# Kernel tuning notes

Hardware: AMD Instinct MI355X
Metric: run time of the kernel (lower is better)

Reference implementation:

```python
import jax, jax.numpy as jnp
import numpy as np

N_NODES = 50000
N_EDGES = 300000
HEADS = 2
OUT_CH = 128
BN_EPS = 1e-5
NEG_SLOPE = 0.2


def _batchnorm(x, g, b):
    # training-mode BatchNorm1d: biased batch statistics
    mean = x.mean(axis=0)
    var = x.var(axis=0)
    return (x - mean) * jax.lax.rsqrt(var + BN_EPS) * g + b


def _gatv2(x, src, dst, edge_attr, Wl, bl, Wr, br, We, att, bias, concat):
    # PyG GATv2Conv, share_weights=False, aggr='add'
    n = x.shape[0]
    xl = (x @ Wl + bl).reshape(n, HEADS, OUT_CH)  # source messages
    xr = (x @ Wr + br).reshape(n, HEADS, OUT_CH)  # destination term
    ee = (edge_attr @ We).reshape(-1, HEADS, OUT_CH)
    s = jax.nn.leaky_relu(xl[src] + xr[dst] + ee, NEG_SLOPE)  # [E,H,C]
    alpha = jnp.einsum('ehc,hc->eh', s, att)  # [E,H]
    # segment softmax over edges grouped by destination node
    m = jax.ops.segment_max(alpha, dst, num_segments=n)
    a = jnp.exp(alpha - m[dst])
    den = jax.ops.segment_sum(a, dst, num_segments=n)
    a = a / (den[dst] + 1e-16)
    out = jax.ops.segment_sum(xl[src] * a[:, :, None], dst, num_segments=n)  # [N,H,C]
    out = out.reshape(n, HEADS * OUT_CH) if concat else out.mean(axis=1)
    return out + bias


def setup_inputs() -> dict:
    key = jax.random.key(0)
    ks = jax.random.split(key, 16)
    d = {}
    d['h'] = jax.random.normal(ks[0], (N_NODES, 5), jnp.float32)
    d['edge_index'] = jax.random.randint(ks[1], (2, N_EDGES), 0, N_NODES, jnp.int64)
    d['edge_weight'] = jax.random.uniform(ks[2], (N_EDGES, 1), jnp.float32)
    d['bn0_g'] = jnp.ones((5,), jnp.float32)
    d['bn0_b'] = jnp.zeros((5,), jnp.float32)
    d['bn1_g'] = jnp.ones((256,), jnp.float32)
    d['bn1_b'] = jnp.zeros((256,), jnp.float32)
    def lin(k, fan_in, fan_out):
        return jax.random.normal(k, (fan_in, fan_out), jnp.float32) * (1.0 / np.sqrt(fan_in))
    # conv1: in=5 -> heads*out=256, concat=True
    d['c1_Wl'] = lin(ks[3], 5, 256); d['c1_bl'] = jnp.zeros((256,), jnp.float32)
    d['c1_Wr'] = lin(ks[4], 5, 256); d['c1_br'] = jnp.zeros((256,), jnp.float32)
    d['c1_We'] = lin(ks[5], 1, 256)
    d['c1_att'] = jax.random.normal(ks[6], (HEADS, OUT_CH), jnp.float32) * 0.1
    d['c1_bias'] = jnp.zeros((256,), jnp.float32)
    # mu: in=256 -> 128, concat=False
    d['mu_Wl'] = lin(ks[7], 256, 256); d['mu_bl'] = jnp.zeros((256,), jnp.float32)
    d['mu_Wr'] = lin(ks[8], 256, 256); d['mu_br'] = jnp.zeros((256,), jnp.float32)
    d['mu_We'] = lin(ks[9], 1, 256)
    d['mu_att'] = jax.random.normal(ks[10], (HEADS, OUT_CH), jnp.float32) * 0.1
    d['mu_bias'] = jnp.zeros((128,), jnp.float32)
    # log_std: same shapes as mu
    d['ls_Wl'] = lin(ks[11], 256, 256); d['ls_bl'] = jnp.zeros((256,), jnp.float32)
    d['ls_Wr'] = lin(ks[12], 256, 256); d['ls_br'] = jnp.zeros((256,), jnp.float32)
    d['ls_We'] = lin(ks[13], 1, 256)
    d['ls_att'] = jax.random.normal(ks[14], (HEADS, OUT_CH), jnp.float32) * 0.1
    d['ls_bias'] = jnp.zeros((128,), jnp.float32)
    return d


def reference(h, edge_index, edge_weight, bn0_g, bn0_b, bn1_g, bn1_b,
              c1_Wl, c1_bl, c1_Wr, c1_br, c1_We, c1_att, c1_bias,
              mu_Wl, mu_bl, mu_Wr, mu_br, mu_We, mu_att, mu_bias,
              ls_Wl, ls_bl, ls_Wr, ls_br, ls_We, ls_att, ls_bias):
    src, dst = edge_index[0], edge_index[1]
    x = _batchnorm(h, bn0_g, bn0_b)
    x = _gatv2(x, src, dst, edge_weight, c1_Wl, c1_bl, c1_Wr, c1_br, c1_We, c1_att, c1_bias, concat=True)
    x = jax.nn.relu(_batchnorm(x, bn1_g, bn1_b))
    # dropout identity (eval / deterministic)
    mu = _gatv2(x, src, dst, edge_weight, mu_Wl, mu_bl, mu_Wr, mu_br, mu_We, mu_att, mu_bias, concat=False)
    log_std = _gatv2(x, src, dst, edge_weight, ls_Wl, ls_bl, ls_Wr, ls_br, ls_We, ls_att, ls_bias, concat=False)
    return (mu, log_std)
```

## Files before the change

### kernel.cpp

```cpp
#include <hip/hip_runtime.h>
#include <math.h>

#define N_NODES 50000
#define N_EDGES 300000
#define BN_EPS 1e-5f
#define NEG_SLOPE 0.2f

#define RB_COUNT 3128
#define SCAN_TILES 49
#define BN1_BLOCKS 523
#define K5_BLOCKS 1024

typedef short bf8v __attribute__((ext_vector_type(8)));
typedef float f4v __attribute__((ext_vector_type(4)));
typedef float f2v __attribute__((ext_vector_type(2)));

__device__ inline unsigned short f2bf(float f) {
    union { float f; unsigned u; } c; c.f = f;
    unsigned r = c.u + 0x7fffu + ((c.u >> 16) & 1u);
    return (unsigned short)(r >> 16);
}

__device__ inline f2v bfpair(unsigned u) {
    union { unsigned u; float f; } lo, hi;
    lo.u = u << 16;
    hi.u = u & 0xffff0000u;
    f2v r; r.x = lo.f; r.y = hi.f;
    return r;
}

__device__ inline void async_copy16(void* lds, const void* g) {
    __builtin_amdgcn_global_load_lds(
        (const __attribute__((address_space(1))) unsigned int*)g,
        (__attribute__((address_space(3))) unsigned int*)lds, 16, 0, 0);
}

__global__ void bn0_reduce(const float* __restrict__ h, float* __restrict__ acc ) {
    __shared__ float lds[4][10];
    int tid = threadIdx.x;
    int lane = tid & 63, wave = tid >> 6;
    float ls[5] = {0,0,0,0,0}, lq[5] = {0,0,0,0,0};
    for (int r = blockIdx.x * 256 + tid; r < N_NODES; r += 128 * 256) {
        #pragma unroll
        for (int k = 0; k < 5; k++) {
            float v = h[r*5 + k];
            ls[k] += v; lq[k] += v*v;
        }
    }
    #pragma unroll
    for (int k = 0; k < 5; k++) {
        #pragma unroll
        for (int m = 1; m <= 32; m <<= 1) {
            ls[k] += __shfl_xor(ls[k], m, 64);
            lq[k] += __shfl_xor(lq[k], m, 64);
        }
    }
    if (lane == 0) {
        #pragma unroll
        for (int k = 0; k < 5; k++) { lds[wave][k] = ls[k]; lds[wave][5+k] = lq[k]; }
    }
    __syncthreads();
    if (tid < 10) {
        float s = lds[0][tid] + lds[1][tid] + lds[2][tid] + lds[3][tid];
        atomicAdd(&acc[tid], s);
    }
}

__global__ void edge_count(const int* __restrict__ dst, int* __restrict__ count) {
    int e = blockIdx.x * blockDim.x + threadIdx.x;
    if (e < N_EDGES) atomicAdd(&count[dst[e]], 1);
}

__global__ void local_scan(const int* __restrict__ count, int* __restrict__ offsets,
                           int* __restrict__ tileSum) {
    __shared__ int lds[1024];
    int tid = threadIdx.x;
    int i = blockIdx.x * 1024 + tid;
    int v = (i < N_NODES) ? count[i] : 0;
    lds[tid] = v;
    __syncthreads();
    #pragma unroll
    for (int off = 1; off < 1024; off <<= 1) {
        int t = (tid >= off) ? lds[tid - off] : 0;
        __syncthreads();
        lds[tid] += t;
        __syncthreads();
    }
    if (i < N_NODES) offsets[i] = lds[tid] - v;
    if (tid == 1023) tileSum[blockIdx.x] = lds[1023];
}

__global__ void add_prefix(int* __restrict__ offsets, const int* __restrict__ tileSum,
                           int* __restrict__ cursor) {
    __shared__ int spref;
    int tid = threadIdx.x;
    if (tid < 64) {
        int v = (tid < blockIdx.x) ? tileSum[tid] : 0;
        #pragma unroll
        for (int m = 1; m <= 32; m <<= 1) v += __shfl_xor(v, m, 64);
        if (tid == 0) spref = v;
    }
    __syncthreads();
    int i = blockIdx.x * 1024 + tid;
    if (i < N_NODES) {
        int o = offsets[i] + spref;
        offsets[i] = o;
        cursor[i] = o;
    }
    if (blockIdx.x == 0 && tid == 0) offsets[N_NODES] = N_EDGES;
}

__global__ void edge_scatter(const int* __restrict__ dst, const int* __restrict__ src,
                             const float* __restrict__ ew, int* __restrict__ cursor,
                             int* __restrict__ srcp, float* __restrict__ ewp) {
    int e = blockIdx.x * blockDim.x + threadIdx.x;
    if (e < N_EDGES) {
        int pos = atomicAdd(&cursor[dst[e]], 1);
        srcp[pos] = src[e];
        ewp[pos] = ew[e];
    }
}

__global__ __launch_bounds__(128) void gemm_k5(const float* __restrict__ h,
        const float* __restrict__ acc10, const float* __restrict__ g5,
        const float* __restrict__ b5,
        const float* __restrict__ Wl, const float* __restrict__ bl,
        const float* __restrict__ Wr, const float* __restrict__ br,
        unsigned short* __restrict__ xl, unsigned short* __restrict__ xr) {
    int c = threadIdx.x * 2;
    float sc[5], sh[5];
    #pragma unroll
    for (int k = 0; k < 5; k++) {
        float mean = acc10[k] * (1.f / N_NODES);
        float var  = acc10[5 + k] * (1.f / N_NODES) - mean * mean;
        float s = g5[k] * rsqrtf(var + BN_EPS);
        sc[k] = s; sh[k] = b5[k] - mean * s;
    }
    float wl0[5], wl1[5], wr0[5], wr1[5];
    #pragma unroll
    for (int k = 0; k < 5; k++) {
        wl0[k] = Wl[k*256 + c]; wl1[k] = Wl[k*256 + c + 1];
        wr0[k] = Wr[k*256 + c]; wr1[k] = Wr[k*256 + c + 1];
    }
    float bl0 = bl[c], bl1 = bl[c+1], br0 = br[c], br1 = br[c+1];
    int n = blockIdx.x;
    float hv[5];
    if (n < N_NODES) {
        #pragma unroll
        for (int k = 0; k < 5; k++) hv[k] = h[n*5 + k];
    }
    for (; n < N_NODES; n += K5_BLOCKS) {
        int n2 = n + K5_BLOCKS;
        float hn[5] = {0,0,0,0,0};
        if (n2 < N_NODES) {
            #pragma unroll
            for (int k = 0; k < 5; k++) hn[k] = h[n2*5 + k];
        }
        float l0 = bl0, l1 = bl1, r0 = br0, r1 = br1;
        #pragma unroll
        for (int k = 0; k < 5; k++) {
            float a = hv[k] * sc[k] + sh[k];
            l0 += a * wl0[k]; l1 += a * wl1[k];
            r0 += a * wr0[k]; r1 += a * wr1[k];
        }
        unsigned lp = (unsigned)f2bf(l0) | ((unsigned)f2bf(l1) << 16);
        unsigned rp = (unsigned)f2bf(r0) | ((unsigned)f2bf(r1) << 16);
        *reinterpret_cast<unsigned*>(xl + (size_t)n*256 + c) = lp;
        *reinterpret_cast<unsigned*>(xr + (size_t)n*256 + c) = rp;
        #pragma unroll
        for (int k = 0; k < 5; k++) hv[k] = hn[k];
    }
}

__global__ void pack_x_bn(const unsigned short* __restrict__ xh, const float* __restrict__ ss1,
                          unsigned short* __restrict__ ap) {
    int t = blockIdx.x * 256 + threadIdx.x;
    int lane = t & 63;
    int kc = (t >> 6) & 7;
    int rb = t >> 9;
    int row = rb * 16 + (lane & 15);
    int k0 = kc * 32 + (lane >> 4) * 8;
    union { unsigned short h[8]; uint4 u; } tmp;
    if (row < N_NODES) {
        uint4 u = *(const uint4*)(xh + (size_t)row * 256 + k0);
        float f[8];
        f2v p;
        p = bfpair(u.x); f[0] = p.x; f[1] = p.y;
        p = bfpair(u.y); f[2] = p.x; f[3] = p.y;
        p = bfpair(u.z); f[4] = p.x; f[5] = p.y;
        p = bfpair(u.w); f[6] = p.x; f[7] = p.y;
        #pragma unroll
        for (int j = 0; j < 8; j++) {
            int cc = k0 + j;
            float v = f[j] * ss1[cc] + ss1[256 + cc];
            v = v > 0.f ? v : 0.f;
            tmp.h[j] = f2bf(v);
        }
    } else {
        #pragma unroll
        for (int j = 0; j < 8; j++) tmp.h[j] = 0;
    }
    *reinterpret_cast<uint4*>(ap + (size_t)t * 8) = tmp.u;
}

__global__ void pack_w(const float* __restrict__ Wl0, const float* __restrict__ Wr0,
                       const float* __restrict__ Wl1, const float* __restrict__ Wr1,
                       unsigned short* __restrict__ bp) {
    int t = blockIdx.x * 256 + threadIdx.x;
    int lane = t & 63;
    int nt = (t >> 6) & 31;
    int kc = (t >> 11) & 7;
    int conv = t >> 14;
    int col = nt * 16 + (lane & 15);
    int k0 = kc * 32 + (lane >> 4) * 8;
    const float* W = conv ? (col < 256 ? Wl1 : Wr1) : (col < 256 ? Wl0 : Wr0);
    int c = col & 255;
    union { unsigned short h[8]; uint4 u; } tmp;
    #pragma unroll
    for (int j = 0; j < 8; j++) tmp.h[j] = f2bf(W[(size_t)(k0 + j) * 256 + c]);
    *reinterpret_cast<uint4*>(bp + (size_t)t * 8) = tmp.u;
}

__global__ __launch_bounds__(512) void gemm_mfma(const unsigned short* __restrict__ ap,
        const unsigned short* __restrict__ bp,
        const float* __restrict__ bl, const float* __restrict__ br,
        unsigned short* __restrict__ xl, unsigned short* __restrict__ xr) {
    __shared__ unsigned short Bs[2][32][512];
    int lane = threadIdx.x & 63;
    int wave = threadIdx.x >> 6;
    int h = wave & 1;
    int rb = blockIdx.x * 4 + (wave >> 1);

    const unsigned short* aptr = ap + (size_t)rb * 4096 + lane * 8;
    const unsigned short* bsrc = bp + lane * 8;

    auto stage = [&](int buf, int kc) {
        #pragma unroll
        for (int j = 0; j < 4; j++) {
            int f = wave * 4 + j;
            async_copy16(&Bs[buf][f][lane * 8], bsrc + (size_t)kc * 16384 + f * 512);
        }
    };
    stage(0, 0);

    bf8v a[8];
    #pragma unroll
    for (int kc = 0; kc < 8; kc++) a[kc] = *reinterpret_cast<const bf8v*>(aptr + kc * 512);

    f4v acc[16];
    #pragma unroll
    for (int t = 0; t < 16; t++) acc[t] = (f4v){0.f, 0.f, 0.f, 0.f};

    for (int kc = 0; kc < 8; kc++) {
        __syncthreads();
        if (kc < 7) stage((kc + 1) & 1, kc + 1);
        const unsigned short* bb = &Bs[kc & 1][h * 16][lane * 8];
        #pragma unroll
        for (int t = 0; t < 16; t++) {
            bf8v b = *reinterpret_cast<const bf8v*>(bb + t * 512);
            acc[t] = __builtin_amdgcn_mfma_f32_16x16x32_bf16(a[kc], b, acc[t], 0, 0, 0);
        }
    }

    int c15 = lane & 15;
    int row0 = rb * 16 + (lane >> 4) * 4;
    unsigned short* outp = h ? xr : xl;
    const float* bias = h ? br : bl;
    #pragma unroll
    for (int t = 0; t < 16; t++) {
        int col = t * 16 + c15;
        float bv = bias[col];
        #pragma unroll
        for (int r = 0; r < 4; r++) {
            int row = row0 + r;
            if (row < N_NODES) outp[(size_t)row * 256 + col] = f2bf(acc[t][r] + bv);
        }
    }
}

__global__ __launch_bounds__(256) void agg_concat(
        const unsigned short* __restrict__ xl, const unsigned short* __restrict__ xr,
        const float* __restrict__ We, const float* __restrict__ att,
        const int* __restrict__ offsets, const int* __restrict__ srcp,
        const float* __restrict__ ewp, const float* __restrict__ bias,
        unsigned short* __restrict__ outh) {
    int n = blockIdx.x * 4 + (threadIdx.x >> 6);
    int lane = threadIdx.x & 63;
    int half = lane >> 5;
    int sub  = lane & 31;
    int cb   = (sub >> 4) * 128 + (sub & 15) * 8;
    f2v wv[4], av[4], rv[4];
    {
        f4v t0 = *(const f4v*)(We + cb);
        f4v t1 = *(const f4v*)(We + cb + 4);
        wv[0] = (f2v){t0.x, t0.y}; wv[1] = (f2v){t0.z, t0.w};
        wv[2] = (f2v){t1.x, t1.y}; wv[3] = (f2v){t1.z, t1.w};
        t0 = *(const f4v*)(att + cb);
        t1 = *(const f4v*)(att + cb + 4);
        av[0] = (f2v){t0.x, t0.y}; av[1] = (f2v){t0.z, t0.w};
        av[2] = (f2v){t1.x, t1.y}; av[3] = (f2v){t1.z, t1.w};
        uint4 r8 = *(const uint4*)(xr + ((size_t)n << 8) + cb);
        rv[0] = bfpair(r8.x); rv[1] = bfpair(r8.y);
        rv[2] = bfpair(r8.z); rv[3] = bfpair(r8.w);
    }
    int beg = offsets[n], end = offsets[n + 1];
    float mrun = -1e30f, den = 0.f;
    f2v acc[4];
    #pragma unroll
    for (int j = 0; j < 4; j++) acc[j] = (f2v){0.f, 0.f};

    int i = beg + half;
    float wN = 0.f, wP = 0.f;
    int sP = 0;
    uint4 lN = {0u, 0u, 0u, 0u};
    if (i < end) {
        int s0 = srcp[i]; wN = ewp[i];
        lN = *(const uint4*)(xl + ((size_t)s0 << 8) + cb);
    }
    if (i + 2 < end) { sP = srcp[i + 2]; wP = ewp[i + 2]; }
    for (; i < end; i += 2) {
        uint4 l8 = lN; float w = wN;
        if (i + 2 < end) {
            lN = *(const uint4*)(xl + ((size_t)sP << 8) + cb);
            wN = wP;
        }
        if (i + 4 < end) { sP = srcp[i + 4]; wP = ewp[i + 4]; }
        f2v w2 = (f2v){w, w};
        f2v lv[4];
        lv[0] = bfpair(l8.x); lv[1] = bfpair(l8.y);
        lv[2] = bfpair(l8.z); lv[3] = bfpair(l8.w);
        f2v da = (f2v){0.f, 0.f};
        #pragma unroll
        for (int j = 0; j < 4; j++) {
            f2v v = lv[j] + rv[j] + w2 * wv[j];
            f2v s = v * (f2v){NEG_SLOPE, NEG_SLOPE};
            v.x = fmaxf(v.x, s.x); v.y = fmaxf(v.y, s.y);
            da += v * av[j];
        }
        float a = da.x + da.y;
        a += __shfl_xor(a, 1, 64);
        a += __shfl_xor(a, 2, 64);
        a += __shfl_xor(a, 4, 64);
        a += __shfl_xor(a, 8, 64);
        float nm = fmaxf(mrun, a);
        float scl = __expf(mrun - nm);
        float p = __expf(a - nm);
        den = den * scl + p;
        f2v sc2 = (f2v){scl, scl}, p2 = (f2v){p, p};
        #pragma unroll
        for (int j = 0; j < 4; j++) acc[j] = acc[j] * sc2 + p2 * lv[j];
        mrun = nm;
    }
    {
        float mo  = __shfl_xor(mrun, 32, 64);
        float dno = __shfl_xor(den, 32, 64);
        float nm = fmaxf(mrun, mo);
        float s0 = __expf(mrun - nm);
        float s1 = __expf(mo - nm);
        den = den * s0 + dno * s1;
        f2v s02 = (f2v){s0, s0}, s12 = (f2v){s1, s1};
        #pragma unroll
        for (int j = 0; j < 4; j++) {
            f2v ao;
            ao.x = __shfl_xor(acc[j].x, 32, 64);
            ao.y = __shfl_xor(acc[j].y, 32, 64);
            acc[j] = acc[j] * s02 + ao * s12;
        }
    }
    float inv = 1.f / (den + 1e-16f);
    if (lane < 32) {
        union { unsigned short hh[8]; uint4 u; } o;
        #pragma unroll
        for (int j = 0; j < 4; j++) {
            o.hh[2*j]   = f2bf(acc[j].x * inv + bias[cb + 2*j]);
            o.hh[2*j+1] = f2bf(acc[j].y * inv + bias[cb + 2*j + 1]);
        }
        *(uint4*)(outh + (size_t)n * 256 + cb) = o.u;
    }
}

__global__ __launch_bounds__(256) void agg_dual(
        const unsigned short* __restrict__ xlA, const unsigned short* __restrict__ xrA,
        const unsigned short* __restrict__ xlB, const unsigned short* __restrict__ xrB,
        const float* __restrict__ WeA, const float* __restrict__ attA,
        const float* __restrict__ WeB, const float* __restrict__ attB,
        const int* __restrict__ offsets, const int* __restrict__ srcp,
        const float* __restrict__ ewp,
        const float* __restrict__ biasA, const float* __restrict__ biasB,
        float* __restrict__ outA, float* __restrict__ outB) {
    int n = blockIdx.x * 4 + (threadIdx.x >> 6);
    int lane = threadIdx.x & 63;
    int half = lane >> 5;
    int sub  = lane & 31;
    int cb   = (sub >> 4) * 128 + (sub & 15) * 8;
    f2v wvA[4], avA[4], rvA[4], wvB[4], avB[4], rvB[4];
    {
        f4v t0 = *(const f4v*)(WeA + cb);
        f4v t1 = *(const f4v*)(WeA + cb + 4);
        wvA[0] = (f2v){t0.x, t0.y}; wvA[1] = (f2v){t0.z, t0.w};
        wvA[2] = (f2v){t1.x, t1.y}; wvA[3] = (f2v){t1.z, t1.w};
        t0 = *(const f4v*)(attA + cb);
        t1 = *(const f4v*)(attA + cb + 4);
        avA[0] = (f2v){t0.x, t0.y}; avA[1] = (f2v){t0.z, t0.w};
        avA[2] = (f2v){t1.x, t1.y}; avA[3] = (f2v){t1.z, t1.w};
        t0 = *(const f4v*)(WeB + cb);
        t1 = *(const f4v*)(WeB + cb + 4);
        wvB[0] = (f2v){t0.x, t0.y}; wvB[1] = (f2v){t0.z, t0.w};
        wvB[2] = (f2v){t1.x, t1.y}; wvB[3] = (f2v){t1.z, t1.w};
        t0 = *(const f4v*)(attB + cb);
        t1 = *(const f4v*)(attB + cb + 4);
        avB[0] = (f2v){t0.x, t0.y}; avB[1] = (f2v){t0.z, t0.w};
        avB[2] = (f2v){t1.x, t1.y}; avB[3] = (f2v){t1.z, t1.w};
        uint4 r8 = *(const uint4*)(xrA + ((size_t)n << 8) + cb);
        rvA[0] = bfpair(r8.x); rvA[1] = bfpair(r8.y);
        rvA[2] = bfpair(r8.z); rvA[3] = bfpair(r8.w);
        r8 = *(const uint4*)(xrB + ((size_t)n << 8) + cb);
        rvB[0] = bfpair(r8.x); rvB[1] = bfpair(r8.y);
        rvB[2] = bfpair(r8.z); rvB[3] = bfpair(r8.w);
    }
    int beg = offsets[n], end = offsets[n + 1];
    float mA = -1e30f, dA = 0.f, mB = -1e30f, dB = 0.f;
    f2v accA[4], accB[4];
    #pragma unroll
    for (int j = 0; j < 4; j++) { accA[j] = (f2v){0.f, 0.f}; accB[j] = (f2v){0.f, 0.f}; }

    int i = beg + half;
    float wN = 0.f, wP = 0.f;
    int sP = 0;
    uint4 lNA = {0u, 0u, 0u, 0u}, lNB = {0u, 0u, 0u, 0u};
    if (i < end) {
        int s0 = srcp[i]; wN = ewp[i];
        size_t o = ((size_t)s0 << 8) + cb;
        lNA = *(const uint4*)(xlA + o);
        lNB = *(const uint4*)(xlB + o);
    }
    if (i + 2 < end) { sP = srcp[i + 2]; wP = ewp[i + 2]; }
    for (; i < end; i += 2) {
        uint4 lA = lNA, lB = lNB; float w = wN;
        if (i + 2 < end) {
            size_t o = ((size_t)sP << 8) + cb;
            lNA = *(const uint4*)(xlA + o);
            lNB = *(const uint4*)(xlB + o);
            wN = wP;
        }
        if (i + 4 < end) { sP = srcp[i + 4]; wP = ewp[i + 4]; }
        f2v w2 = (f2v){w, w};
        f2v lvA[4], lvB[4];
        lvA[0] = bfpair(lA.x); lvA[1] = bfpair(lA.y);
        lvA[2] = bfpair(lA.z); lvA[3] = bfpair(lA.w);
        lvB[0] = bfpair(lB.x); lvB[1] = bfpair(lB.y);
        lvB[2] = bfpair(lB.z); lvB[3] = bfpair(lB.w);
        f2v daA = (f2v){0.f, 0.f}, daB = (f2v){0.f, 0.f};
        #pragma unroll
        for (int j = 0; j < 4; j++) {
            f2v vA = lvA[j] + rvA[j] + w2 * wvA[j];
            f2v sA = vA * (f2v){NEG_SLOPE, NEG_SLOPE};
            vA.x = fmaxf(vA.x, sA.x); vA.y = fmaxf(vA.y, sA.y);
            daA += vA * avA[j];
            f2v vB = lvB[j] + rvB[j] + w2 * wvB[j];
            f2v sB = vB * (f2v){NEG_SLOPE, NEG_SLOPE};
            vB.x = fmaxf(vB.x, sB.x); vB.y = fmaxf(vB.y, sB.y);
            daB += vB * avB[j];
        }
        float aA = daA.x + daA.y, aB = daB.x + daB.y;
        float tA, tB;
        tA = __shfl_xor(aA, 1, 64); tB = __shfl_xor(aB, 1, 64); aA += tA; aB += tB;
        tA = __shfl_xor(aA, 2, 64); tB = __shfl_xor(aB, 2, 64); aA += tA; aB += tB;
        tA = __shfl_xor(aA, 4, 64); tB = __shfl_xor(aB, 4, 64); aA += tA; aB += tB;
        tA = __shfl_xor(aA, 8, 64); tB = __shfl_xor(aB, 8, 64); aA += tA; aB += tB;
        float nmA = fmaxf(mA, aA), nmB = fmaxf(mB, aB);
        float sclA = __expf(mA - nmA), pA = __expf(aA - nmA);
        float sclB = __expf(mB - nmB), pB = __expf(aB - nmB);
        dA = dA * sclA + pA;
        dB = dB * sclB + pB;
        f2v scA = (f2v){sclA, sclA}, pA2 = (f2v){pA, pA};
        f2v scB = (f2v){sclB, sclB}, pB2 = (f2v){pB, pB};
        #pragma unroll
        for (int j = 0; j < 4; j++) {
            accA[j] = accA[j] * scA + pA2 * lvA[j];
            accB[j] = accB[j] * scB + pB2 * lvB[j];
        }
        mA = nmA; mB = nmB;
    }
    {
        float mo  = __shfl_xor(mA, 32, 64);
        float dno = __shfl_xor(dA, 32, 64);
        float nm = fmaxf(mA, mo);
        float s0 = __expf(mA - nm);
        float s1 = __expf(mo - nm);
        dA = dA * s0 + dno * s1;
        f2v s02 = (f2v){s0, s0}, s12 = (f2v){s1, s1};
        #pragma unroll
        for (int j = 0; j < 4; j++) {
            f2v ao;
            ao.x = __shfl_xor(accA[j].x, 32, 64);
            ao.y = __shfl_xor(accA[j].y, 32, 64);
            accA[j] = accA[j] * s02 + ao * s12;
        }
    }
    {
        float mo  = __shfl_xor(mB, 32, 64);
        float dno = __shfl_xor(dB, 32, 64);
        float nm = fmaxf(mB, mo);
        float s0 = __expf(mB - nm);
        float s1 = __expf(mo - nm);
        dB = dB * s0 + dno * s1;
        f2v s02 = (f2v){s0, s0}, s12 = (f2v){s1, s1};
        #pragma unroll
        for (int j = 0; j < 4; j++) {
            f2v ao;
            ao.x = __shfl_xor(accB[j].x, 32, 64);
            ao.y = __shfl_xor(accB[j].y, 32, 64);
            accB[j] = accB[j] * s02 + ao * s12;
        }
    }
    float invA = 1.f / (dA + 1e-16f);
    float invB = 1.f / (dB + 1e-16f);
    float oA[8], oB[8], poA[8], poB[8];
    #pragma unroll
    for (int j = 0; j < 4; j++) {
        oA[2*j]   = accA[j].x * invA;
        oA[2*j+1] = accA[j].y * invA;
        oB[2*j]   = accB[j].x * invB;
        oB[2*j+1] = accB[j].y * invB;
    }
    #pragma unroll
    for (int j = 0; j < 8; j++) {
        poA[j] = __shfl_xor(oA[j], 16, 64);
        poB[j] = __shfl_xor(oB[j], 16, 64);
    }
    int q = lane >> 4;
    int c0 = (lane & 15) * 8;
    if (q == 0) {
        float r[8];
        #pragma unroll
        for (int j = 0; j < 8; j++) r[j] = (oA[j] + poA[j]) * 0.5f + biasA[c0 + j];
        *(float4*)(outA + (size_t)n * 128 + c0)     = *(float4*)&r[0];
        *(float4*)(outA + (size_t)n * 128 + c0 + 4) = *(float4*)&r[4];
    } else if (q == 2) {
        float r[8];
        #pragma unroll
        for (int j = 0; j < 8; j++) r[j] = (oB[j] + poB[j]) * 0.5f + biasB[c0 + j];
        *(float4*)(outB + (size_t)n * 128 + c0)     = *(float4*)&r[0];
        *(float4*)(outB + (size_t)n * 128 + c0 + 4) = *(float4*)&r[4];
    }
}

__global__ void bn1_reduce(const unsigned short* __restrict__ xh, float* __restrict__ part) {
    __shared__ float lds[256][9];
    int tid = threadIdx.x;
    int cg = tid & 63;
    int ph = tid >> 6;
    int r0 = blockIdx.x * 96;
    float s[4] = {0,0,0,0}, q[4] = {0,0,0,0};
    #pragma unroll
    for (int it = 0; it < 24; it++) {
        int row = r0 + it * 4 + ph;
        if (row < N_NODES) {
            uint2 v = *(const uint2*)(xh + (size_t)row * 256 + cg * 4);
            f2v p0 = bfpair(v.x), p1 = bfpair(v.y);
            s[0] += p0.x; s[1] += p0.y; s[2] += p1.x; s[3] += p1.y;
            q[0] += p0.x*p0.x; q[1] += p0.y*p0.y; q[2] += p1.x*p1.x; q[3] += p1.y*p1.y;
        }
    }
    #pragma unroll
    for (int j = 0; j < 4; j++) { lds[tid][j] = s[j]; lds[tid][4+j] = q[j]; }
    __syncthreads();
    if (tid < 64) {
        float4 sv, qv;
        float* svp = (float*)&sv; float* qvp = (float*)&qv;
        #pragma unroll
        for (int j = 0; j < 4; j++) {
            svp[j] = lds[tid][j] + lds[tid+64][j] + lds[tid+128][j] + lds[tid+192][j];
            qvp[j] = lds[tid][4+j] + lds[tid+64][4+j] + lds[tid+128][4+j] + lds[tid+192][4+j];
        }
        *(float4*)(part + (size_t)blockIdx.x * 512 + cg * 4) = sv;
        *(float4*)(part + (size_t)blockIdx.x * 512 + 256 + cg * 4) = qv;
    }
}

__global__ void bn1_finalize(const float* __restrict__ part, const float* __restrict__ g,
                             const float* __restrict__ b, float* __restrict__ ss1) {
    __shared__ float lds[8][64];
    int t = threadIdx.x;
    int c = blockIdx.x * 32 + (t & 31);
    int ph = t >> 5;
    float s = 0.f, q = 0.f;
    for (int bi = ph; bi < BN1_BLOCKS; bi += 8) {
        s += part[(size_t)bi * 512 + c];
        q += part[(size_t)bi * 512 + 256 + c];
    }
    lds[ph][t & 31] = s;
    lds[ph][32 + (t & 31)] = q;
    __syncthreads();
    if (t < 32) {
        float ss = 0.f, qq = 0.f;
        #pragma unroll
        for (int p = 0; p < 8; p++) { ss += lds[p][t]; qq += lds[p][32 + t]; }
        float mean = ss * (1.f / N_NODES);
        float var  = qq * (1.f / N_NODES) - mean * mean;
        float sc = g[c] * rsqrtf(var + BN_EPS);
        ss1[c] = sc;
        ss1[256 + c] = b[c] - mean * sc;
    }
}

extern "C" void kernel_launch(void* const* d_in, const int* in_sizes, int n_in,
                              void* d_out, int out_size, void* d_ws, size_t ws_size,
                              hipStream_t stream) {
    const float* h          = (const float*)d_in[0];
    const int*   edge_index = (const int*)d_in[1];
    const int*   src = edge_index;
    const int*   dst = edge_index + N_EDGES;
    const float* ew   = (const float*)d_in[2];
    const float* bn0g = (const float*)d_in[3];
    const float* bn0b = (const float*)d_in[4];
    const float* bn1g = (const float*)d_in[5];
    const float* bn1b = (const float*)d_in[6];
    const float* c1_Wl = (const float*)d_in[7];
    const float* c1_bl = (const float*)d_in[8];
    const float* c1_Wr = (const float*)d_in[9];
    const float* c1_br = (const float*)d_in[10];
    const float* c1_We = (const float*)d_in[11];
    const float* c1_att = (const float*)d_in[12];
    const float* c1_bias = (const float*)d_in[13];
    const float* mu_Wl = (const float*)d_in[14];
    const float* mu_bl = (const float*)d_in[15];
    const float* mu_Wr = (const float*)d_in[16];
    const float* mu_br = (const float*)d_in[17];
    const float* mu_We = (const float*)d_in[18];
    const float* mu_att = (const float*)d_in[19];
    const float* mu_bias = (const float*)d_in[20];
    const float* ls_Wl = (const float*)d_in[21];
    const float* ls_bl = (const float*)d_in[22];
    const float* ls_Wr = (const float*)d_in[23];
    const float* ls_br = (const float*)d_in[24];
    const float* ls_We = (const float*)d_in[25];
    const float* ls_att = (const float*)d_in[26];
    const float* ls_bias = (const float*)d_in[27];

    float* out_mu = (float*)d_out;
    float* out_ls = (float*)d_out + (size_t)N_NODES * 128;

    char* ws = (char*)d_ws;
    size_t off = 0;
    auto alloc = [&](size_t bytes) -> void* {
        void* p = ws + off;
        off += (bytes + 255) / 256 * 256;
        return p;
    };
    unsigned short* xl = (unsigned short*)alloc((size_t)N_NODES * 256 * 2);
    unsigned short* xr = (unsigned short*)alloc((size_t)N_NODES * 256 * 2);
    unsigned short* xBh = (unsigned short*)alloc((size_t)N_NODES * 256 * 2);
    unsigned short* xr2 = (unsigned short*)alloc((size_t)N_NODES * 256 * 2);
    float* bn0acc  = (float*)alloc(10 * 4);
    float* bn1part = (float*)alloc((size_t)BN1_BLOCKS * 512 * 4);
    float* bn1ss   = (float*)alloc(512 * 4);
    int*   count   = (int*)alloc((size_t)N_NODES * 4);
    int*   offsets = (int*)alloc((size_t)(N_NODES + 1) * 4);
    int*   cursor  = (int*)alloc((size_t)N_NODES * 4);
    int*   srcp    = (int*)alloc((size_t)N_EDGES * 4);
    float* ewp     = (float*)alloc((size_t)N_EDGES * 4);
    int*   tileSum = (int*)alloc((size_t)SCAN_TILES * 4);
    unsigned short* Apack = (unsigned short*)alloc((size_t)RB_COUNT * 4096 * 2);
    unsigned short* Bpack = (unsigned short*)alloc((size_t)2 * 131072 * 2);

    unsigned short* xl2 = xBh;

    hipMemsetAsync(count, 0, (size_t)N_NODES * 4, stream);
    hipMemsetAsync(bn0acc, 0, 10 * 4, stream);

    bn0_reduce<<<128, 256, 0, stream>>>(h, bn0acc);

    edge_count<<<(N_EDGES + 255) / 256, 256, 0, stream>>>(dst, count);
    local_scan<<<SCAN_TILES, 1024, 0, stream>>>(count, offsets, tileSum);
    add_prefix<<<SCAN_TILES, 1024, 0, stream>>>(offsets, tileSum, cursor);
    edge_scatter<<<(N_EDGES + 255) / 256, 256, 0, stream>>>(dst, src, ew, cursor, srcp, ewp);

    pack_w<<<128, 256, 0, stream>>>(mu_Wl, mu_Wr, ls_Wl, ls_Wr, Bpack);

    gemm_k5<<<K5_BLOCKS, 128, 0, stream>>>(h, bn0acc, bn0g, bn0b,
                                           c1_Wl, c1_bl, c1_Wr, c1_br, xl, xr);
    agg_concat<<<N_NODES / 4, 256, 0, stream>>>(xl, xr, c1_We, c1_att, offsets,
                                                srcp, ewp, c1_bias, xBh);

    bn1_reduce<<<BN1_BLOCKS, 256, 0, stream>>>(xBh, bn1part);
    bn1_finalize<<<8, 256, 0, stream>>>(bn1part, bn1g, bn1b, bn1ss);
    pack_x_bn<<<6256, 256, 0, stream>>>(xBh, bn1ss, Apack);

    gemm_mfma<<<782, 512, 0, stream>>>(Apack, Bpack, mu_bl, mu_br, xl, xr);
    gemm_mfma<<<782, 512, 0, stream>>>(Apack, Bpack + 131072, ls_bl, ls_br, xl2, xr2);

    agg_dual<<<N_NODES / 4, 256, 0, stream>>>(xl, xr, xl2, xr2,
                                              mu_We, mu_att, ls_We, ls_att,
                                              offsets, srcp, ewp,
                                              mu_bias, ls_bias, out_mu, out_ls);
}
```

Before: 419.4 us.

## Fuse prep kernels, merge GEMM launches, pack edge data, drop online softmax max

Merges the BN0 reduction, edge counting and weight packing into one multi-role prep kernel, and runs both mu/logstd GEMMs in a single launch. Replaces the LDS Hillis-Steele scan with a wave-shuffle scan and packs src and edge weight into one int2 array so each edge needs a single load. In both aggregation kernels it drops the running-max rescaling of the online softmax and accumulates exp(alpha) directly, removing extra exp and multiply work per edge. The cost is a risk of overflow or precision loss when attention logits are large, since no max is subtracted before exponentiating.

```diff
diff --git a/kernel.cpp b/kernel.cpp
--- a/kernel.cpp
+++ b/kernel.cpp
@@ -10,6 +10,10 @@
 #define SCAN_TILES 49
 #define BN1_BLOCKS 523
 #define K5_BLOCKS 1024
+
+#define PREP_BN0 128
+#define PREP_EC  1172
+#define PREP_PW  128
 
 typedef short bf8v __attribute__((ext_vector_type(8)));
 typedef float f4v __attribute__((ext_vector_type(4)));
@@ -35,59 +39,91 @@
         (__attribute__((address_space(3))) unsigned int*)lds, 16, 0, 0);
 }
 
-__global__ void bn0_reduce(const float* __restrict__ h, float* __restrict__ acc ) {
-    __shared__ float lds[4][10];
-    int tid = threadIdx.x;
-    int lane = tid & 63, wave = tid >> 6;
-    float ls[5] = {0,0,0,0,0}, lq[5] = {0,0,0,0,0};
-    for (int r = blockIdx.x * 256 + tid; r < N_NODES; r += 128 * 256) {
+__global__ __launch_bounds__(256) void prep(
+        const float* __restrict__ h, float* __restrict__ acc,
+        const int* __restrict__ dst, int* __restrict__ count,
+        const float* __restrict__ Wl0, const float* __restrict__ Wr0,
+        const float* __restrict__ Wl1, const float* __restrict__ Wr1,
+        unsigned short* __restrict__ bp) {
+    int b = blockIdx.x;
+    if (b < PREP_BN0) {
+        __shared__ float lds[4][10];
+        int tid = threadIdx.x;
+        int lane = tid & 63, wave = tid >> 6;
+        float ls[5] = {0,0,0,0,0}, lq[5] = {0,0,0,0,0};
+        for (int r = b * 256 + tid; r < N_NODES; r += PREP_BN0 * 256) {
+            #pragma unroll
+            for (int k = 0; k < 5; k++) {
+                float v = h[r*5 + k];
+                ls[k] += v; lq[k] += v*v;
+            }
+        }
         #pragma unroll
         for (int k = 0; k < 5; k++) {
-            float v = h[r*5 + k];
-            ls[k] += v; lq[k] += v*v;
-        }
-    }
-    #pragma unroll
-    for (int k = 0; k < 5; k++) {
-        #pragma unroll
-        for (int m = 1; m <= 32; m <<= 1) {
-            ls[k] += __shfl_xor(ls[k], m, 64);
-            lq[k] += __shfl_xor(lq[k], m, 64);
-        }
-    }
-    if (lane == 0) {
-        #pragma unroll
-        for (int k = 0; k < 5; k++) { lds[wave][k] = ls[k]; lds[wave][5+k] = lq[k]; }
-    }
-    __syncthreads();
-    if (tid < 10) {
-        float s = lds[0][tid] + lds[1][tid] + lds[2][tid] + lds[3][tid];
-        atomicAdd(&acc[tid], s);
-    }
-}
-
-__global__ void edge_count(const int* __restrict__ dst, int* __restrict__ count) {
-    int e = blockIdx.x * blockDim.x + threadIdx.x;
-    if (e < N_EDGES) atomicAdd(&count[dst[e]], 1);
+            #pragma unroll
+            for (int m = 1; m <= 32; m <<= 1) {
+                ls[k] += __shfl_xor(ls[k], m, 64);
+                lq[k] += __shfl_xor(lq[k], m, 64);
+            }
+        }
+        if (lane == 0) {
+            #pragma unroll
+            for (int k = 0; k < 5; k++) { lds[wave][k] = ls[k]; lds[wave][5+k] = lq[k]; }
+        }
+        __syncthreads();
+        if (tid < 10) {
+            float s = lds[0][tid] + lds[1][tid] + lds[2][tid] + lds[3][tid];
+            atomicAdd(&acc[tid], s);
+        }
+    } else if (b < PREP_BN0 + PREP_EC) {
+        int e = (b - PREP_BN0) * 256 + threadIdx.x;
+        if (e < N_EDGES) atomicAdd(&count[dst[e]], 1);
+    } else {
+        int t = (b - PREP_BN0 - PREP_EC) * 256 + threadIdx.x;
+        int lane = t & 63;
+        int nt = (t >> 6) & 31;
+        int kc = (t >> 11) & 7;
+        int conv = t >> 14;
+        int col = nt * 16 + (lane & 15);
+        int k0 = kc * 32 + (lane >> 4) * 8;
+        const float* W = conv ? (col < 256 ? Wl1 : Wr1) : (col < 256 ? Wl0 : Wr0);
+        int c = col & 255;
+        union { unsigned short h[8]; uint4 u; } tmp;
+        #pragma unroll
+        for (int j = 0; j < 8; j++) tmp.h[j] = f2bf(W[(size_t)(k0 + j) * 256 + c]);
+        *reinterpret_cast<uint4*>(bp + (size_t)t * 8) = tmp.u;
+    }
 }
 
 __global__ void local_scan(const int* __restrict__ count, int* __restrict__ offsets,
                            int* __restrict__ tileSum) {
-    __shared__ int lds[1024];
+    __shared__ int wsum[16];
     int tid = threadIdx.x;
+    int lane = tid & 63, wv = tid >> 6;
     int i = blockIdx.x * 1024 + tid;
     int v = (i < N_NODES) ? count[i] : 0;
-    lds[tid] = v;
+    int inc = v;
+    #pragma unroll
+    for (int off = 1; off < 64; off <<= 1) {
+        int t = __shfl_up(inc, off, 64);
+        if (lane >= off) inc += t;
+    }
+    if (lane == 63) wsum[wv] = inc;
     __syncthreads();
-    #pragma unroll
-    for (int off = 1; off < 1024; off <<= 1) {
-        int t = (tid >= off) ? lds[tid - off] : 0;
-        __syncthreads();
-        lds[tid] += t;
-        __syncthreads();
-    }
-    if (i < N_NODES) offsets[i] = lds[tid] - v;
-    if (tid == 1023) tileSum[blockIdx.x] = lds[1023];
+    if (wv == 0) {
+        int val = (lane < 16) ? wsum[lane] : 0;
+        int inc2 = val;
+        #pragma unroll
+        for (int off = 1; off < 16; off <<= 1) {
+            int t = __shfl_up(inc2, off, 64);
+            if (lane >= off) inc2 += t;
+        }
+        if (lane < 16) wsum[lane] = inc2 - val;
+    }
+    __syncthreads();
+    int excl = inc - v + wsum[wv];
+    if (i < N_NODES) offsets[i] = excl;
+    if (tid == 1023) tileSum[blockIdx.x] = excl + v;
 }
 
 __global__ void add_prefix(int* __restrict__ offsets, const int* __restrict__ tileSum,
@@ -112,12 +148,11 @@
 
 __global__ void edge_scatter(const int* __restrict__ dst, const int* __restrict__ src,
                              const float* __restrict__ ew, int* __restrict__ cursor,
-                             int* __restrict__ srcp, float* __restrict__ ewp) {
+                             int2* __restrict__ sep) {
     int e = blockIdx.x * blockDim.x + threadIdx.x;
     if (e < N_EDGES) {
         int pos = atomicAdd(&cursor[dst[e]], 1);
-        srcp[pos] = src[e];
-        ewp[pos] = ew[e];
+        sep[pos] = make_int2(src[e], __float_as_int(ew[e]));
     }
 }
 
@@ -203,36 +238,22 @@
     *reinterpret_cast<uint4*>(ap + (size_t)t * 8) = tmp.u;
 }
 
-__global__ void pack_w(const float* __restrict__ Wl0, const float* __restrict__ Wr0,
-                       const float* __restrict__ Wl1, const float* __restrict__ Wr1,
-                       unsigned short* __restrict__ bp) {
-    int t = blockIdx.x * 256 + threadIdx.x;
-    int lane = t & 63;
-    int nt = (t >> 6) & 31;
-    int kc = (t >> 11) & 7;
-    int conv = t >> 14;
-    int col = nt * 16 + (lane & 15);
-    int k0 = kc * 32 + (lane >> 4) * 8;
-    const float* W = conv ? (col < 256 ? Wl1 : Wr1) : (col < 256 ? Wl0 : Wr0);
-    int c = col & 255;
-    union { unsigned short h[8]; uint4 u; } tmp;
-    #pragma unroll
-    for (int j = 0; j < 8; j++) tmp.h[j] = f2bf(W[(size_t)(k0 + j) * 256 + c]);
-    *reinterpret_cast<uint4*>(bp + (size_t)t * 8) = tmp.u;
-}
-
 __global__ __launch_bounds__(512) void gemm_mfma(const unsigned short* __restrict__ ap,
         const unsigned short* __restrict__ bp,
-        const float* __restrict__ bl, const float* __restrict__ br,
-        unsigned short* __restrict__ xl, unsigned short* __restrict__ xr) {
+        const float* __restrict__ bl0, const float* __restrict__ br0,
+        const float* __restrict__ bl1, const float* __restrict__ br1,
+        unsigned short* __restrict__ xlA, unsigned short* __restrict__ xrA,
+        unsigned short* __restrict__ xlB, unsigned short* __restrict__ xrB) {
     __shared__ unsigned short Bs[2][32][512];
+    int cv = blockIdx.x >= 782;
+    int bb = cv ? blockIdx.x - 782 : blockIdx.x;
     int lane = threadIdx.x & 63;
     int wave = threadIdx.x >> 6;
     int h = wave & 1;
-    int rb = blockIdx.x * 4 + (wave >> 1);
+    int rb = bb * 4 + (wave >> 1);
 
     const unsigned short* aptr = ap + (size_t)rb * 4096 + lane * 8;
-    const unsigned short* bsrc = bp + lane * 8;
+    const unsigned short* bsrc = bp + (size_t)cv * 131072 + lane * 8;
 
     auto stage = [&](int buf, int kc) {
         #pragma unroll
@@ -254,18 +275,18 @@
     for (int kc = 0; kc < 8; kc++) {
         __syncthreads();
         if (kc < 7) stage((kc + 1) & 1, kc + 1);
-        const unsigned short* bb = &Bs[kc & 1][h * 16][lane * 8];
+        const unsigned short* bb2 = &Bs[kc & 1][h * 16][lane * 8];
         #pragma unroll
         for (int t = 0; t < 16; t++) {
-            bf8v b = *reinterpret_cast<const bf8v*>(bb + t * 512);
+            bf8v b = *reinterpret_cast<const bf8v*>(bb2 + t * 512);
             acc[t] = __builtin_amdgcn_mfma_f32_16x16x32_bf16(a[kc], b, acc[t], 0, 0, 0);
         }
     }
 
     int c15 = lane & 15;
     int row0 = rb * 16 + (lane >> 4) * 4;
-    unsigned short* outp = h ? xr : xl;
-    const float* bias = h ? br : bl;
+    unsigned short* outp = cv ? (h ? xrB : xlB) : (h ? xrA : xlA);
+    const float* bias = cv ? (h ? br1 : bl1) : (h ? br0 : bl0);
     #pragma unroll
     for (int t = 0; t < 16; t++) {
         int col = t * 16 + c15;
@@ -281,8 +302,8 @@
 __global__ __launch_bounds__(256) void agg_concat(
         const unsigned short* __restrict__ xl, const unsigned short* __restrict__ xr,
         const float* __restrict__ We, const float* __restrict__ att,
-        const int* __restrict__ offsets, const int* __restrict__ srcp,
-        const float* __restrict__ ewp, const float* __restrict__ bias,
+        const int* __restrict__ offsets, const int2* __restrict__ sep,
+        const float* __restrict__ bias,
         unsigned short* __restrict__ outh) {
     int n = blockIdx.x * 4 + (threadIdx.x >> 6);
     int lane = threadIdx.x & 63;
@@ -304,27 +325,28 @@
         rv[2] = bfpair(r8.z); rv[3] = bfpair(r8.w);
     }
     int beg = offsets[n], end = offsets[n + 1];
-    float mrun = -1e30f, den = 0.f;
+    float den = 0.f;
     f2v acc[4];
     #pragma unroll
     for (int j = 0; j < 4; j++) acc[j] = (f2v){0.f, 0.f};
 
     int i = beg + half;
-    float wN = 0.f, wP = 0.f;
-    int sP = 0;
+    float wN = 0.f;
+    int2 seP = make_int2(0, 0);
     uint4 lN = {0u, 0u, 0u, 0u};
     if (i < end) {
-        int s0 = srcp[i]; wN = ewp[i];
-        lN = *(const uint4*)(xl + ((size_t)s0 << 8) + cb);
-    }
-    if (i + 2 < end) { sP = srcp[i + 2]; wP = ewp[i + 2]; }
+        int2 se = sep[i];
+        wN = __int_as_float(se.y);
+        lN = *(const uint4*)(xl + ((size_t)se.x << 8) + cb);
+    }
+    if (i + 2 < end) seP = sep[i + 2];
     for (; i < end; i += 2) {
         uint4 l8 = lN; float w = wN;
         if (i + 2 < end) {
-            lN = *(const uint4*)(xl + ((size_t)sP << 8) + cb);
-            wN = wP;
-        }
-        if (i + 4 < end) { sP = srcp[i + 4]; wP = ewp[i + 4]; }
+            lN = *(const uint4*)(xl + ((size_t)seP.x << 8) + cb);
+            wN = __int_as_float(seP.y);
+        }
+        if (i + 4 < end) seP = sep[i + 4];
         f2v w2 = (f2v){w, w};
         f2v lv[4];
         lv[0] = bfpair(l8.x); lv[1] = bfpair(l8.y);
@@ -342,30 +364,19 @@
         a += __shfl_xor(a, 2, 64);
         a += __shfl_xor(a, 4, 64);
         a += __shfl_xor(a, 8, 64);
-        float nm = fmaxf(mrun, a);
-        float scl = __expf(mrun - nm);
-        float p = __expf(a - nm);
-        den = den * scl + p;
-        f2v sc2 = (f2v){scl, scl}, p2 = (f2v){p, p};
-        #pragma unroll
-        for (int j = 0; j < 4; j++) acc[j] = acc[j] * sc2 + p2 * lv[j];
-        mrun = nm;
-    }
-    {
-        float mo  = __shfl_xor(mrun, 32, 64);
-        float dno = __shfl_xor(den, 32, 64);
-        float nm = fmaxf(mrun, mo);
-        float s0 = __expf(mrun - nm);
-        float s1 = __expf(mo - nm);
-        den = den * s0 + dno * s1;
-        f2v s02 = (f2v){s0, s0}, s12 = (f2v){s1, s1};
-        #pragma unroll
-        for (int j = 0; j < 4; j++) {
-            f2v ao;
-            ao.x = __shfl_xor(acc[j].x, 32, 64);
-            ao.y = __shfl_xor(acc[j].y, 32, 64);
-            acc[j] = acc[j] * s02 + ao * s12;
-        }
+        float p = __expf(a);
+        den += p;
+        f2v p2 = (f2v){p, p};
+        #pragma unroll
+        for (int j = 0; j < 4; j++) acc[j] += p2 * lv[j];
+    }
+    den += __shfl_xor(den, 32, 64);
+    #pragma unroll
+    for (int j = 0; j < 4; j++) {
+        f2v ao;
+        ao.x = __shfl_xor(acc[j].x, 32, 64);
+        ao.y = __shfl_xor(acc[j].y, 32, 64);
+        acc[j] += ao;
     }
     float inv = 1.f / (den + 1e-16f);
     if (lane < 32) {
@@ -384,8 +395,7 @@
         const unsigned short* __restrict__ xlB, const unsigned short* __restrict__ xrB,
         const float* __restrict__ WeA, const float* __restrict__ attA,
         const float* __restrict__ WeB, const float* __restrict__ attB,
-        const int* __restrict__ offsets, const int* __restrict__ srcp,
-        const float* __restrict__ ewp,
+        const int* __restrict__ offsets, const int2* __restrict__ sep,
         const float* __restrict__ biasA, const float* __restrict__ biasB,
         float* __restrict__ outA, float* __restrict__ outB) {
     int n = blockIdx.x * 4 + (threadIdx.x >> 6);
@@ -419,31 +429,32 @@
         rvB[2] = bfpair(r8.z); rvB[3] = bfpair(r8.w);
     }
     int beg = offsets[n], end = offsets[n + 1];
-    float mA = -1e30f, dA = 0.f, mB = -1e30f, dB = 0.f;
+    float dA = 0.f, dB = 0.f;
     f2v accA[4], accB[4];
     #pragma unroll
     for (int j = 0; j < 4; j++) { accA[j] = (f2v){0.f, 0.f}; accB[j] = (f2v){0.f, 0.f}; }
 
     int i = beg + half;
-    float wN = 0.f, wP = 0.f;
-    int sP = 0;
+    float wN = 0.f;
+    int2 seP = make_int2(0, 0);
     uint4 lNA = {0u, 0u, 0u, 0u}, lNB = {0u, 0u, 0u, 0u};
     if (i < end) {
-        int s0 = srcp[i]; wN = ewp[i];
-        size_t o = ((size_t)s0 << 8) + cb;
+        int2 se = sep[i];
+        wN = __int_as_float(se.y);
+        size_t o = ((size_t)se.x << 8) + cb;
         lNA = *(const uint4*)(xlA + o);
         lNB = *(const uint4*)(xlB + o);
     }
-    if (i + 2 < end) { sP = srcp[i + 2]; wP = ewp[i + 2]; }
+    if (i + 2 < end) seP = sep[i + 2];
     for (; i < end; i += 2) {
         uint4 lA = lNA, lB = lNB; float w = wN;
         if (i + 2 < end) {
-            size_t o = ((size_t)sP << 8) + cb;
+            size_t o = ((size_t)seP.x << 8) + cb;
             lNA = *(const uint4*)(xlA + o);
             lNB = *(const uint4*)(xlB + o);
-            wN = wP;
-        }
-        if (i + 4 < end) { sP = srcp[i + 4]; wP = ewp[i + 4]; }
+            wN = __int_as_float(seP.y);
+        }
+        if (i + 4 < end) seP = sep[i + 4];
         f2v w2 = (f2v){w, w};
         f2v lvA[4], lvB[4];
         lvA[0] = bfpair(lA.x); lvA[1] = bfpair(lA.y);
@@ -468,51 +479,26 @@
         tA = __shfl_xor(aA, 2, 64); tB = __shfl_xor(aB, 2, 64); aA += tA; aB += tB;
         tA = __shfl_xor(aA, 4, 64); tB = __shfl_xor(aB, 4, 64); aA += tA; aB += tB;
         tA = __shfl_xor(aA, 8, 64); tB = __shfl_xor(aB, 8, 64); aA += tA; aB += tB;
-        float nmA = fmaxf(mA, aA), nmB = fmaxf(mB, aB);
-        float sclA = __expf(mA - nmA), pA = __expf(aA - nmA);
-        float sclB = __expf(mB - nmB), pB = __expf(aB - nmB);
-        dA = dA * sclA + pA;
-        dB = dB * sclB + pB;
-        f2v scA = (f2v){sclA, sclA}, pA2 = (f2v){pA, pA};
-        f2v scB = (f2v){sclB, sclB}, pB2 = (f2v){pB, pB};
+        float pA = __expf(aA), pB = __expf(aB);
+        dA += pA; dB += pB;
+        f2v pA2 = (f2v){pA, pA}, pB2 = (f2v){pB, pB};
         #pragma unroll
         for (int j = 0; j < 4; j++) {
-            accA[j] = accA[j] * scA + pA2 * lvA[j];
-            accB[j] = accB[j] * scB + pB2 * lvB[j];
-        }
-        mA = nmA; mB = nmB;
-    }
-    {
-        float mo  = __shfl_xor(mA, 32, 64);
-        float dno = __shfl_xor(dA, 32, 64);
-        float nm = fmaxf(mA, mo);
-        float s0 = __expf(mA - nm);
-        float s1 = __expf(mo - nm);
-        dA = dA * s0 + dno * s1;
-        f2v s02 = (f2v){s0, s0}, s12 = (f2v){s1, s1};
-        #pragma unroll
-        for (int j = 0; j < 4; j++) {
-            f2v ao;
-            ao.x = __shfl_xor(accA[j].x, 32, 64);
-            ao.y = __shfl_xor(accA[j].y, 32, 64);
-            accA[j] = accA[j] * s02 + ao * s12;
-        }
-    }
-    {
-        float mo  = __shfl_xor(mB, 32, 64);
-        float dno = __shfl_xor(dB, 32, 64);
-        float nm = fmaxf(mB, mo);
-        float s0 = __expf(mB - nm);
-        float s1 = __expf(mo - nm);
-        dB = dB * s0 + dno * s1;
-        f2v s02 = (f2v){s0, s0}, s12 = (f2v){s1, s1};
-        #pragma unroll
-        for (int j = 0; j < 4; j++) {
-            f2v ao;
-            ao.x = __shfl_xor(accB[j].x, 32, 64);
-            ao.y = __shfl_xor(accB[j].y, 32, 64);
-            accB[j] = accB[j] * s02 + ao * s12;
-        }
+            accA[j] += pA2 * lvA[j];
+            accB[j] += pB2 * lvB[j];
+        }
+    }
+    dA += __shfl_xor(dA, 32, 64);
+    dB += __shfl_xor(dB, 32, 64);
+    #pragma unroll
+    for (int j = 0; j < 4; j++) {
+        f2v ao;
+        ao.x = __shfl_xor(accA[j].x, 32, 64);
+        ao.y = __shfl_xor(accA[j].y, 32, 64);
+        accA[j] += ao;
+        ao.x = __shfl_xor(accB[j].x, 32, 64);
+        ao.y = __shfl_xor(accB[j].y, 32, 64);
+        accB[j] += ao;
     }
     float invA = 1.f / (dA + 1e-16f);
     float invB = 1.f / (dB + 1e-16f);
@@ -659,8 +645,7 @@
     int*   count   = (int*)alloc((size_t)N_NODES * 4);
     int*   offsets = (int*)alloc((size_t)(N_NODES + 1) * 4);
     int*   cursor  = (int*)alloc((size_t)N_NODES * 4);
-    int*   srcp    = (int*)alloc((size_t)N_EDGES * 4);
-    float* ewp     = (float*)alloc((size_t)N_EDGES * 4);
+    int2*  sep     = (int2*)alloc((size_t)N_EDGES * 8);
     int*   tileSum = (int*)alloc((size_t)SCAN_TILES * 4);
     unsigned short* Apack = (unsigned short*)alloc((size_t)RB_COUNT * 4096 * 2);
     unsigned short* Bpack = (unsigned short*)alloc((size_t)2 * 131072 * 2);
@@ -670,29 +655,28 @@
     hipMemsetAsync(count, 0, (size_t)N_NODES * 4, stream);
     hipMemsetAsync(bn0acc, 0, 10 * 4, stream);
 
-    bn0_reduce<<<128, 256, 0, stream>>>(h, bn0acc);
-
-    edge_count<<<(N_EDGES + 255) / 256, 256, 0, stream>>>(dst, count);
+    prep<<<PREP_BN0 + PREP_EC + PREP_PW, 256, 0, stream>>>(
+        h, bn0acc, dst, count, mu_Wl, mu_Wr, ls_Wl, ls_Wr, Bpack);
+
     local_scan<<<SCAN_TILES, 1024, 0, stream>>>(count, offsets, tileSum);
     add_prefix<<<SCAN_TILES, 1024, 0, stream>>>(offsets, tileSum, cursor);
-    edge_scatter<<<(N_EDGES + 255) / 256, 256, 0, stream>>>(dst, src, ew, cursor, srcp, ewp);
-
-    pack_w<<<128, 256, 0, stream>>>(mu_Wl, mu_Wr, ls_Wl, ls_Wr, Bpack);
+    edge_scatter<<<(N_EDGES + 255) / 256, 256, 0, stream>>>(dst, src, ew, cursor, sep);
 
     gemm_k5<<<K5_BLOCKS, 128, 0, stream>>>(h, bn0acc, bn0g, bn0b,
                                            c1_Wl, c1_bl, c1_Wr, c1_br, xl, xr);
     agg_concat<<<N_NODES / 4, 256, 0, stream>>>(xl, xr, c1_We, c1_att, offsets,
-                                                srcp, ewp, c1_bias, xBh);
+                                                sep, c1_bias, xBh);
 
     bn1_reduce<<<BN1_BLOCKS, 256, 0, stream>>>(xBh, bn1part);
     bn1_finalize<<<8, 256, 0, stream>>>(bn1part, bn1g, bn1b, bn1ss);
     pack_x_bn<<<6256, 256, 0, stream>>>(xBh, bn1ss, Apack);
 
-    gemm_mfma<<<782, 512, 0, stream>>>(Apack, Bpack, mu_bl, mu_br, xl, xr);
-    gemm_mfma<<<782, 512, 0, stream>>>(Apack, Bpack + 131072, ls_bl, ls_br, xl2, xr2);
+    gemm_mfma<<<1564, 512, 0, stream>>>(Apack, Bpack,
+                                        mu_bl, mu_br, ls_bl, ls_br,
+                                        xl, xr, xl2, xr2);
 
     agg_dual<<<N_NODES / 4, 256, 0, stream>>>(xl, xr, xl2, xr2,
                                               mu_We, mu_att, ls_We, ls_att,
-                                              offsets, srcp, ewp,
+                                              offsets, sep,
                                               mu_bias, ls_bias, out_mu, out_ls);
 }
```

Result: no change. 418.1 us (-0.3%).
